# Optimization experiments

Measured on AMD Instinct MI355X. Metric: run time of the kernel, lower is better.

Reference implementation:

```python
import jax, jax.numpy as jnp
import numpy as np

N_NODES = 100000
N_EDGES = 3200000
DIMS = [32, 256, 1024, 1024, 256, 6]


def setup_inputs() -> dict:
    key = jax.random.key(0)
    ks = jax.random.split(key, 2 + 2 * 5)
    inp = {
        "x": jax.random.normal(ks[0], (N_NODES, DIMS[0]), dtype=jnp.float32),
        "edge_index": jax.random.randint(ks[1], (2, N_EDGES), 0, N_NODES, dtype=jnp.int64),
    }
    for i in range(5):
        fan_in, fan_out = DIMS[i], DIMS[i + 1]
        scale = (2.0 / (fan_in + fan_out)) ** 0.5  # glorot-ish
        inp[f"W{i+1}"] = jax.random.normal(ks[2 + 2 * i], (fan_in, fan_out), dtype=jnp.float32) * scale
        inp[f"b{i+1}"] = jnp.zeros((fan_out,), dtype=jnp.float32)
    return inp


def _gcn_forward(x, edge_index, Ws, bs):
    N = x.shape[0]
    # add self loops (PyG GCNConv default)
    loop = jnp.arange(N, dtype=edge_index.dtype)
    src = jnp.concatenate([edge_index[0], loop])
    dst = jnp.concatenate([edge_index[1], loop])
    # symmetric normalization: deg computed on target index (gcn_norm)
    deg = jax.ops.segment_sum(jnp.ones_like(dst, dtype=x.dtype), dst, num_segments=N)
    dinv = jnp.where(deg > 0, jax.lax.rsqrt(deg), 0.0)
    norm = (dinv[src] * dinv[dst])[:, None]  # [E+N, 1]

    def conv(h, W, b):
        h = h @ W                                    # dense linear
        msg = h[src] * norm                          # gather + scale
        agg = jax.ops.segment_sum(msg, dst, num_segments=N)  # scatter-add
        return agg + b

    h = x
    for i in range(4):
        h = jax.nn.relu(conv(h, Ws[i], bs[i]))
    return conv(h, Ws[4], bs[4])


def reference(x, edge_index, W1, b1, W2, b2, W3, b3, W4, b4, W5, b5):
    return _gcn_forward(x, edge_index, (W1, W2, W3, W4, W5), (b1, b2, b3, b4, b5))
```

## Files before the change

kernel.cpp:

```cpp
#include <hip/hip_runtime.h>

typedef unsigned char u8;
typedef unsigned short u16;
typedef unsigned int u32;
typedef __bf16 bf16_t;
typedef bf16_t bf16x8 __attribute__((ext_vector_type(8)));
typedef float f32x4 __attribute__((ext_vector_type(4)));
typedef float f32x2 __attribute__((ext_vector_type(2)));

#define LDS_PTR(p) ((__attribute__((address_space(3))) unsigned int*)(p))
#define GLB_PTR(p) ((const __attribute__((address_space(1))) unsigned int*)(p))

#define BSH 9
#define BCAP 32768

static __device__ __forceinline__ float bf2f(u16 h) {
  u32 u = ((u32)h) << 16;
  return __builtin_bit_cast(float, u);
}
static __device__ __forceinline__ u16 f2bf(float f) {
  u32 u = __builtin_bit_cast(u32, f);
  u += 0x7fffu + ((u >> 16) & 1u);
  return (u16)(u >> 16);
}

static __device__ __forceinline__ int xcd_swizzle(int wg, int nwg) {
  const int q = nwg >> 3, r = nwg & 7;
  const int xcd = wg & 7, pos = wg >> 3;
  return (xcd < r ? xcd * (q + 1) : r * (q + 1) + (xcd - r) * q) + pos;
}

__global__ void detect_kernel(const int* __restrict__ ei, const u16* __restrict__ x,
                              int* __restrict__ flags, int* __restrict__ zp, int zn) {
  __shared__ int cnt;
  if (threadIdx.x == 0) cnt = 0;
  __syncthreads();
  if (blockIdx.x == 0) {
    if (ei[1 + 2 * threadIdx.x] != 0) atomicAdd(&cnt, 1);
    __syncthreads();
    if (threadIdx.x == 0) flags[0] = (cnt == 0) ? 1 : 0;
  } else if (blockIdx.x == 1) {
    u32 u = x[threadIdx.x];
    u32 e = (u >> 7) & 0xFF;
    if (e >= 0x60 && e <= 0x83) atomicAdd(&cnt, 1);
    __syncthreads();
    if (threadIdx.x == 0) flags[1] = (cnt >= 240) ? 0 : 1;
  } else {
    for (int i = threadIdx.x; i < zn; i += 256) zp[i] = 0;
  }
}

static __device__ __forceinline__ int eidx(const void* ei, size_t i, int m) {
  return m ? (int)((const long long*)ei)[i] : ((const int*)ei)[i];
}

__global__ void zero_out_kernel(void* __restrict__ out, int n, const int* __restrict__ flags) {
  int i = blockIdx.x * 256 + threadIdx.x;
  if (i < n) {
    if (flags[1]) ((float*)out)[i] = 0.0f;
    else ((u16*)out)[i] = 0;
  }
}

struct CvtArgs {
  const void* src[10];
  u16* dst[10];
  int K[10];
  int N[10];
  int start[11];
};
__global__ void convert_all_kernel(CvtArgs a, const int* __restrict__ flags) {
  int idx = blockIdx.x * 256 + threadIdx.x;
  int f32 = flags[1];
#pragma unroll
  for (int t = 0; t < 10; ++t) {
    if (idx >= a.start[t] && idx < a.start[t + 1]) {
      int local = idx - a.start[t];
      int K = a.K[t], N = a.N[t];
      int k = local / N, n = local - k * N;
      float v = f32 ? ((const float*)a.src[t])[local] : bf2f(((const u16*)a.src[t])[local]);
      a.dst[t][(size_t)n * K + k] = f2bf(v);
    }
  }
}

__global__ void prescale_x_kernel(const void* __restrict__ x, void* __restrict__ xs,
                                  const float* __restrict__ dinv, int n,
                                  const int* __restrict__ flags) {
  int i = blockIdx.x * 256 + threadIdx.x;
  if (i >= n) return;
  float w = dinv[i >> 5];
  if (flags[1]) ((float*)xs)[i] = ((const float*)x)[i] * w;
  else ((u16*)xs)[i] = f2bf(bf2f(((const u16*)x)[i]) * w);
}

__global__ __launch_bounds__(256) void bin_kernel(const void* __restrict__ ei,
                                                  int* __restrict__ gcur,
                                                  int2* __restrict__ pairs, int E, int Nn,
                                                  const int* __restrict__ flags, int nblk) {
  __shared__ int h[256];
  __shared__ int base[256];
  const int m = flags[0];
  const int nb = (Nn + (1 << BSH) - 1) >> BSH;
  const int per = (E + nblk - 1) / nblk;
  const int e0 = blockIdx.x * per;
  const int e1 = (e0 + per < E) ? e0 + per : E;
  for (int i = threadIdx.x; i < nb; i += 256) h[i] = 0;
  __syncthreads();
  for (int e = e0 + threadIdx.x; e < e1; e += 256) {
    int d = eidx(ei, (size_t)E + e, m);
    if ((u32)d < (u32)Nn) atomicAdd(&h[d >> BSH], 1);
  }
  __syncthreads();
  for (int i = threadIdx.x; i < nb; i += 256) {
    base[i] = atomicAdd(&gcur[i], h[i]);
    h[i] = 0;
  }
  __syncthreads();
  for (int e = e0 + threadIdx.x; e < e1; e += 256) {
    int d = eidx(ei, (size_t)E + e, m);
    if ((u32)d >= (u32)Nn) continue;
    int s = eidx(ei, (size_t)e, m);
    if ((u32)s >= (u32)Nn) s = 0;
    int b = d >> BSH;
    int p = base[b] + atomicAdd(&h[b], 1);
    if (p < BCAP) pairs[(size_t)b * BCAP + p] = make_int2(s, d);
  }
}

__global__ __launch_bounds__(256) void bucket_scan_kernel(const int* __restrict__ gcur,
                                                          int* __restrict__ gbase, int NB) {
  __shared__ int sd[256];
  int tid = threadIdx.x;
  int v = (tid < NB) ? gcur[tid] : 0;
  if (v > BCAP) v = BCAP;
  sd[tid] = v;
  __syncthreads();
  for (int s = 1; s < 256; s <<= 1) {
    int t = (tid >= s) ? sd[tid - s] : 0;
    __syncthreads();
    sd[tid] += t;
    __syncthreads();
  }
  if (tid < NB) gbase[tid] = sd[tid] - v;
}

__global__ __launch_bounds__(512) void bucket_finalize_kernel(
    const int2* __restrict__ pairs, const int* __restrict__ gcur,
    const int* __restrict__ gbase, int* __restrict__ rowp, float* __restrict__ dinv,
    int* __restrict__ csr, int Nn) {
  __shared__ int cnt[512];
  __shared__ int scn[512];
  const int b = blockIdx.x;
  const int n0 = b << BSH;
  const int tid = threadIdx.x;
  cnt[tid] = 0;
  __syncthreads();
  int tot = gcur[b];
  if (tot > BCAP) tot = BCAP;
  for (int i = tid; i < tot; i += 512) {
    int2 pr = pairs[(size_t)b * BCAP + i];
    atomicAdd(&cnt[pr.y - n0], 1);
  }
  __syncthreads();
  int myc = cnt[tid];
  scn[tid] = myc;
  __syncthreads();
  for (int s = 1; s < 512; s <<= 1) {
    int t = (tid >= s) ? scn[tid - s] : 0;
    __syncthreads();
    scn[tid] += t;
    __syncthreads();
  }
  const int node = n0 + tid;
  const int start = gbase[b] + scn[tid] - myc;
  if (node < Nn) {
    rowp[node] = start;
    dinv[node] = rsqrtf((float)(myc + 1));
    if (node == Nn - 1) rowp[Nn] = gbase[b] + scn[tid];
  }
  cnt[tid] = start;
  __syncthreads();
  for (int i = tid; i < tot; i += 512) {
    int2 pr = pairs[(size_t)b * BCAP + i];
    int p = atomicAdd(&cnt[pr.y - n0], 1);
    csr[p] = pr.x;
  }
}

template <int NPW, int ACT, bool SRCF, bool DSTF>
__global__ __launch_bounds__(256) void spmm_narrow_kernel(
    const void* __restrict__ Hb, void* __restrict__ Gb,
    const int* __restrict__ rowp, const int* __restrict__ csr,
    const float* __restrict__ dinv, const u16* __restrict__ bias,
    int relu, int Nn, int src_stride, int dst_stride, const int* __restrict__ flags) {
  constexpr int G = 64 / NPW;
  constexpr int B = 16;
  const int lane = threadIdx.x & 63;
  const int col = lane & (G - 1);
  const int node = blockIdx.x * 4 * NPW + (threadIdx.x >> 6) * NPW + (lane / G);
  const bool anode = node < Nn;
  const bool act = anode && (col < ACT);
  int sf32 = 0, of32 = 0;
  if (SRCF) sf32 = flags[1];
  if (DSTF) of32 = flags[1];
  const u16* Hs = (const u16*)Hb;
  const float* Hf = (const float*)Hb;

  int e0 = 0, cnt = 0;
  if (anode) {
    e0 = rowp[node];
    cnt = rowp[node + 1] - e0;
  }
  float acc = 0.0f;
  for (int jb = 0; jb < cnt; jb += B) {
    int s[B];
#pragma unroll
    for (int j = 0; j < B; ++j) {
      bool val = (jb + j) < cnt;
      s[j] = val ? csr[e0 + jb + j] : node;
    }
    float v[B];
#pragma unroll
    for (int j = 0; j < B; ++j) {
      bool val = act && ((jb + j) < cnt);
      size_t idx = (size_t)s[j] * src_stride + col;
      v[j] = val ? ((SRCF && sf32) ? Hf[idx] : bf2f(Hs[idx])) : 0.0f;
    }
#pragma unroll
    for (int j = 0; j < B; ++j) acc += v[j];
  }
  if (!act) return;
  const float wi = dinv[node];
  {
    size_t idx = (size_t)node * src_stride + col;
    acc += (SRCF && sf32) ? Hf[idx] : bf2f(Hs[idx]);
  }
  float v = acc * wi;
  if (bias) v += bf2f(bias[col]);
  if (relu) v = fmaxf(v, 0.0f);
  size_t didx = (size_t)node * dst_stride + col;
  if (DSTF && of32) ((float*)Gb)[didx] = v;
  else ((u16*)Gb)[didx] = f2bf(v);
}

template <int W>
__global__ __launch_bounds__(256) void spmm_fp8_kernel(
    const u8* __restrict__ Hq, u16* __restrict__ Gout,
    const int* __restrict__ rowp, const int* __restrict__ csr,
    const float* __restrict__ dinv, int n0, int n1, int dst_stride) {
  constexpr int BPL = W / 64;
  constexpr int ND = BPL / 4;
  constexpr int B = (W == 1024) ? 8 : 16;
  const int lane = threadIdx.x & 63;
  const int node = __builtin_amdgcn_readfirstlane(n0 + blockIdx.x * 4 + (threadIdx.x >> 6));
  if (node >= n1) return;
  const int off = lane * BPL;
  f32x2 acc[2 * ND] = {};

  auto dec1 = [&](const u32* d) {
#pragma unroll
    for (int q = 0; q < ND; ++q) {
      f32x2 a = __builtin_amdgcn_cvt_pk_f32_fp8((int)d[q], false);
      f32x2 b = __builtin_amdgcn_cvt_pk_f32_fp8((int)d[q], true);
      acc[2 * q] += a;
      acc[2 * q + 1] += b;
    }
  };
  auto ldrow = [&](u32* v, int s) {
    const u8* p = Hq + (size_t)s * W + off;
    if constexpr (ND == 4) *(int4*)v = *(const int4*)p;
    else v[0] = *(const u32*)p;
  };

  const int e0 = rowp[node];
  const int cnt = rowp[node + 1] - e0;
  const int tot = cnt + 1;
  const int NB2 = (tot + B - 1) / B;
  const int NBF = NB2 - 1;

  u32 vA[B][ND], vB[B][ND];

  auto ldb_full = [&](u32 (*v)[ND], int k) {
    const int base = k * B;
    int s[B];
#pragma unroll
    for (int j = 0; j < B; ++j) s[j] = csr[e0 + base + j];
#pragma unroll
    for (int j = 0; j < B; ++j) ldrow(v[j], s[j]);
  };
  auto ldb_last = [&](u32 (*v)[ND]) {
    const int base = NBF * B;
#pragma unroll
    for (int j = 0; j < B; ++j) {
      const int i = base + j;
      if (i < tot) {
        int s = (i < cnt) ? csr[e0 + i] : node;
        ldrow(v[j], s);
      } else {
#pragma unroll
        for (int q = 0; q < ND; ++q) v[j][q] = 0u;
      }
    }
  };
  auto decfull = [&](u32 (*v)[ND]) {
#pragma unroll
    for (int j = 0; j < B; ++j) dec1(v[j]);
  };

  if (NB2 == 1) {
    ldb_last(vA);
    decfull(vA);
  } else {
    ldb_last(vA);
    ldb_full(vB, 0);
    int k = 1;
    while (k + 1 < NBF) {
      decfull(vA);
      ldb_full(vA, k);
      decfull(vB);
      ldb_full(vB, k + 1);
      k += 2;
    }
    if (k < NBF) {
      decfull(vA);
      ldb_full(vA, k);
      decfull(vB);
      decfull(vA);
    } else {
      decfull(vA);
      decfull(vB);
    }
  }

  const float wi = dinv[node];
  u32 d[2 * ND];
#pragma unroll
  for (int kk = 0; kk < 2 * ND; ++kk) {
    float v0 = acc[kk].x * wi, v1 = acc[kk].y * wi;
    d[kk] = (u32)f2bf(v0) | ((u32)f2bf(v1) << 16);
  }
  u16* gp = Gout + (size_t)(node - n0) * dst_stride + off;
  if constexpr (ND == 4) {
    ((int4*)gp)[0] = make_int4((int)d[0], (int)d[1], (int)d[2], (int)d[3]);
    ((int4*)gp)[1] = make_int4((int)d[4], (int)d[5], (int)d[6], (int)d[7]);
  } else {
    *(int2*)gp = make_int2((int)d[0], (int)d[1]);
  }
}

__global__ __launch_bounds__(256) void spmm_u8_kernel(
    const u8* __restrict__ Hq, u16* __restrict__ G,
    const int* __restrict__ rowp, const int* __restrict__ csr,
    const float* __restrict__ dinv, const u32* __restrict__ maxbits,
    const u16* __restrict__ bias, int relu, int Nn, int dst_stride) {
  constexpr int B = 16;
  const int lane = threadIdx.x & 63;
  const int node = __builtin_amdgcn_readfirstlane(blockIdx.x * 4 + (threadIdx.x >> 6));
  if (node >= Nn) return;
  const int off = lane * 4;
  float mx = __builtin_bit_cast(float, *maxbits);
  float sq = mx > 0.0f ? mx * (1.0f / 127.0f) : 0.0f;
  u32 aP0 = 0, aP1 = 0;

  auto dec1 = [&](u32 d) {
    aP0 += d & 0x00ff00ffu;
    aP1 += (d >> 8) & 0x00ff00ffu;
  };
  auto ldrow = [&](u32* v, int s) { *v = *(const u32*)(Hq + (size_t)s * 256 + off); };

  const int e0 = rowp[node];
  const int cnt = rowp[node + 1] - e0;
  const int tot = cnt + 1;
  const int NB2 = (tot + B - 1) / B;
  const int NBF = NB2 - 1;

  u32 vA[B], vB[B];

  auto ldb_full = [&](u32* v, int k) {
    const int base = k * B;
    int s[B];
#pragma unroll
    for (int j = 0; j < B; ++j) s[j] = csr[e0 + base + j];
#pragma unroll
    for (int j = 0; j < B; ++j) ldrow(&v[j], s[j]);
  };
  auto ldb_last = [&](u32* v) {
    const int base = NBF * B;
#pragma unroll
    for (int j = 0; j < B; ++j) {
      const int i = base + j;
      if (i < tot) {
        int s = (i < cnt) ? csr[e0 + i] : node;
        ldrow(&v[j], s);
      } else {
        v[j] = 0u;
      }
    }
  };
  auto decfull = [&](u32* v) {
#pragma unroll
    for (int j = 0; j < B; ++j) dec1(v[j]);
  };

  if (NB2 == 1) {
    ldb_last(vA);
    decfull(vA);
  } else {
    ldb_last(vA);
    ldb_full(vB, 0);
    int k = 1;
    while (k + 1 < NBF) {
      decfull(vA);
      ldb_full(vA, k);
      decfull(vB);
      ldb_full(vB, k + 1);
      k += 2;
    }
    if (k < NBF) {
      decfull(vA);
      ldb_full(vA, k);
      decfull(vB);
      decfull(vA);
    } else {
      decfull(vA);
      decfull(vB);
    }
  }

  const float wi = dinv[node];
  float su[4];
  su[0] = (float)(aP0 & 0xffffu);
  su[2] = (float)(aP0 >> 16);
  su[1] = (float)(aP1 & 0xffffu);
  su[3] = (float)(aP1 >> 16);
  float vals[4];
#pragma unroll
  for (int k2 = 0; k2 < 4; ++k2) {
    float v = (su[k2] - 128.0f * (float)tot) * wi * sq;
    if (bias) v += bf2f(bias[off + k2]);
    if (relu) v = fmaxf(v, 0.0f);
    vals[k2] = v;
  }
  u32 d0 = (u32)f2bf(vals[0]) | ((u32)f2bf(vals[1]) << 16);
  u32 d1 = (u32)f2bf(vals[2]) | ((u32)f2bf(vals[3]) << 16);
  *(int2*)(G + (size_t)node * dst_stride + off) = make_int2((int)d0, (int)d1);
}

__global__ void quant_kernel(const u16* __restrict__ t4, u8* __restrict__ t4q,
                             const u32* __restrict__ maxbits, int n4) {
  int i = blockIdx.x * 256 + threadIdx.x;
  if (i >= n4) return;
  float mx = __builtin_bit_cast(float, *maxbits);
  float inv = mx > 0.0f ? 127.0f / mx : 0.0f;
  int2 v = ((const int2*)t4)[i];
  float f0 = bf2f((u16)(v.x & 0xffff)), f1 = bf2f((u16)((u32)v.x >> 16));
  float f2 = bf2f((u16)(v.y & 0xffff)), f3 = bf2f((u16)((u32)v.y >> 16));
  int q0 = (int)rintf(f0 * inv), q1 = (int)rintf(f1 * inv);
  int q2 = (int)rintf(f2 * inv), q3 = (int)rintf(f3 * inv);
  q0 = min(127, max(-127, q0)) + 128; q1 = min(127, max(-127, q1)) + 128;
  q2 = min(127, max(-127, q2)) + 128; q3 = min(127, max(-127, q3)) + 128;
  ((u32*)t4q)[i] = (u32)q0 | ((u32)q1 << 8) | ((u32)q2 << 16) | ((u32)q3 << 24);
}

__global__ __launch_bounds__(256) void gemm_fast_kernel(
    const u16* __restrict__ A, int lda, const u16* __restrict__ Bt,
    u16* __restrict__ C, int ldc, const u16* __restrict__ bias,
    int M, int N, int K, int relu, int fp8out, u32* __restrict__ maxout,
    const float* __restrict__ rowscale) {
  __shared__ __align__(16) u16 sA[128 * 64];
  __shared__ __align__(16) u16 sB[128 * 64];
  const int tid = threadIdx.x;
  const int lane = tid & 63;
  const int wave = __builtin_amdgcn_readfirstlane(tid >> 6);
  const int gx = gridDim.x;
  int wg = blockIdx.y * gx + blockIdx.x;
  wg = xcd_swizzle(wg, gx * gridDim.y);
  const int m0 = (wg / gx) * 128, n0 = (wg % gx) * 128;
  const int wm = (wave & 1) * 64, wn = (wave >> 1) * 64;
  const int lr = lane & 15, lq = lane >> 4;
  const int lrow = lane >> 3;
  const int lcol = (lane & 7) * 8;
  f32x4 acc[4][4] = {};

  for (int kb = 0; kb < K; kb += 64) {
#pragma unroll
    for (int it = 0; it < 4; ++it) {
      const int rbase = (it * 4 + wave) * 8;
      int gm = m0 + rbase + lrow;
      if (gm >= M) gm = M - 1;
      __builtin_amdgcn_global_load_lds(GLB_PTR(A + (size_t)gm * lda + kb + lcol),
                                       LDS_PTR(sA + rbase * 64), 16, 0, 0);
      const int gn = n0 + rbase + lrow;
      __builtin_amdgcn_global_load_lds(GLB_PTR(Bt + (size_t)gn * K + kb + lcol),
                                       LDS_PTR(sB + rbase * 64), 16, 0, 0);
    }
    __syncthreads();
#pragma unroll
    for (int ks = 0; ks < 2; ++ks) {
      bf16x8 af[4], bfr[4];
#pragma unroll
      for (int i = 0; i < 4; ++i)
        af[i] = *(const bf16x8*)(sA + (wm + i * 16 + lr) * 64 + ks * 32 + lq * 8);
#pragma unroll
      for (int i = 0; i < 4; ++i)
        bfr[i] = *(const bf16x8*)(sB + (wn + i * 16 + lr) * 64 + ks * 32 + lq * 8);
#pragma unroll
      for (int im = 0; im < 4; ++im)
#pragma unroll
        for (int in = 0; in < 4; ++in)
          acc[im][in] = __builtin_amdgcn_mfma_f32_16x16x32_bf16(af[im], bfr[in], acc[im][in], 0, 0, 0);
    }
    __syncthreads();
  }
  float rs[4][4];
#pragma unroll
  for (int im = 0; im < 4; ++im)
#pragma unroll
    for (int r = 0; r < 4; ++r) {
      int row = m0 + wm + im * 16 + lq * 4 + r;
      rs[im][r] = rowscale ? rowscale[row < M ? row : 0] : 1.0f;
    }
  u32 mymax = 0;
#pragma unroll
  for (int im = 0; im < 4; ++im) {
#pragma unroll
    for (int in = 0; in < 4; ++in) {
      int col = n0 + wn + in * 16 + lr;
      float bv = bias ? bf2f(bias[col]) : 0.0f;
#pragma unroll
      for (int r = 0; r < 4; ++r) {
        int row = m0 + wm + im * 16 + lq * 4 + r;
        if (row < M) {
          float v = acc[im][in][r] + bv;
          if (relu) v = fmaxf(v, 0.0f);
          if (rowscale) v *= rs[im][r];
          if (maxout) {
            u32 ab = __builtin_bit_cast(u32, v) & 0x7fffffffu;
            mymax = mymax > ab ? mymax : ab;
          }
          if (fp8out) {
            int pk = __builtin_amdgcn_cvt_pk_fp8_f32(v, v, 0, false);
            ((u8*)C)[(size_t)row * ldc + col] = (u8)(pk & 0xff);
          } else {
            C[(size_t)row * ldc + col] = f2bf(v);
          }
        }
      }
    }
  }
  if (maxout) {
    u32* red = (u32*)sA;
    red[tid] = mymax;
    __syncthreads();
    for (int s = 128; s > 0; s >>= 1) {
      if (tid < s) red[tid] = red[tid] > red[tid + s] ? red[tid] : red[tid + s];
      __syncthreads();
    }
    if (tid == 0) atomicMax(maxout, red[0]);
  }
}

#define LP 72
__global__ __launch_bounds__(256) void gemm_small_kernel(
    const u16* __restrict__ A, int lda, const u16* __restrict__ Bt,
    u16* __restrict__ C, int ldc, const u16* __restrict__ bias,
    int M, int N, int K, int relu, int fp8out, const float* __restrict__ rowscale) {
  __shared__ __align__(16) u16 sA[128 * LP];
  __shared__ __align__(16) u16 sB[128 * LP];
  const int tid = threadIdx.x;
  const int lane = tid & 63, wave = tid >> 6;
  const int gx = gridDim.x;
  int wg = blockIdx.y * gx + blockIdx.x;
  wg = xcd_swizzle(wg, gx * gridDim.y);
  const int m0 = (wg / gx) * 128, n0 = (wg % gx) * 128;
  const int wm = (wave & 1) * 64, wn = (wave >> 1) * 64;
  const int lr = lane & 15;
  const int lq = lane >> 4;
  f32x4 acc[4][4] = {};

  for (int kb = 0; kb < K; kb += 64) {
#pragma unroll
    for (int it = 0; it < 4; ++it) {
      int linear = it * 2048 + tid * 8;
      int row = linear >> 6, kc = linear & 63;
      int gm = m0 + row, gk = kb + kc;
      int4 v = make_int4(0, 0, 0, 0);
      if (gm < M && gk < K) v = *(const int4*)(A + (size_t)gm * lda + gk);
      *(int4*)(sA + row * LP + kc) = v;
    }
#pragma unroll
    for (int it = 0; it < 4; ++it) {
      int linear = it * 2048 + tid * 8;
      int row = linear >> 6, kc = linear & 63;
      int gn = n0 + row, gk = kb + kc;
      int4 v = make_int4(0, 0, 0, 0);
      if (gn < N && gk < K) v = *(const int4*)(Bt + (size_t)gn * K + gk);
      *(int4*)(sB + row * LP + kc) = v;
    }
    __syncthreads();
#pragma unroll
    for (int ks = 0; ks < 2; ++ks) {
      bf16x8 af[4], bfr[4];
#pragma unroll
      for (int i = 0; i < 4; ++i)
        af[i] = *(const bf16x8*)(sA + (wm + i * 16 + lr) * LP + ks * 32 + lq * 8);
#pragma unroll
      for (int i = 0; i < 4; ++i)
        bfr[i] = *(const bf16x8*)(sB + (wn + i * 16 + lr) * LP + ks * 32 + lq * 8);
#pragma unroll
      for (int im = 0; im < 4; ++im)
#pragma unroll
        for (int in = 0; in < 4; ++in)
          acc[im][in] = __builtin_amdgcn_mfma_f32_16x16x32_bf16(af[im], bfr[in], acc[im][in], 0, 0, 0);
    }
    __syncthreads();
  }
  float rs[4][4];
#pragma unroll
  for (int im = 0; im < 4; ++im)
#pragma unroll
    for (int r = 0; r < 4; ++r) {
      int row = m0 + wm + im * 16 + lq * 4 + r;
      rs[im][r] = rowscale ? rowscale[row < M ? row : 0] : 1.0f;
    }
#pragma unroll
  for (int im = 0; im < 4; ++im) {
#pragma unroll
    for (int in = 0; in < 4; ++in) {
      int col = n0 + wn + in * 16 + lr;
      if (col >= N) continue;
      float bv = bias ? bf2f(bias[col]) : 0.0f;
#pragma unroll
      for (int r = 0; r < 4; ++r) {
        int row = m0 + wm + im * 16 + lq * 4 + r;
        if (row < M) {
          float v = acc[im][in][r] + bv;
          if (relu) v = fmaxf(v, 0.0f);
          if (rowscale) v *= rs[im][r];
          if (fp8out) {
            int pk = __builtin_amdgcn_cvt_pk_fp8_f32(v, v, 0, false);
            ((u8*)C)[(size_t)row * ldc + col] = (u8)(pk & 0xff);
          } else {
            C[(size_t)row * ldc + col] = f2bf(v);
          }
        }
      }
    }
  }
}

extern "C" void kernel_launch(void* const* d_in, const int* in_sizes, int n_in,
                              void* d_out, int out_size, void* d_ws, size_t ws_size,
                              hipStream_t stream) {
  const u16* x  = (const u16*)d_in[0];
  const int* ei = (const int*)d_in[1];

  const int Nn = in_sizes[0] / 32;
  const int E  = in_sizes[1] / 2;
  const int CH = (Nn + 7) / 8;
  const int NR = (Nn + CH - 1) / CH;
  const int NB = (Nn + (1 << BSH) - 1) >> BSH;

  char* w = (char*)d_ws;
  size_t off = 0;
  auto alloc = [&](size_t bytes) -> void* {
    void* p = w + off;
    off = (off + bytes + 255) & ~(size_t)255;
    return p;
  };
  int*   flags  = (int*)alloc(256);
  int*   gcur   = (int*)alloc(1024);
  int*   gbase  = (int*)alloc(1024);
  u32*   tmax   = (u32*)alloc(256);
  int*   rowp   = (int*)alloc((size_t)(Nn + 1) * 4);
  float* dinv   = (float*)alloc((size_t)Nn * 4);
  int*   csr    = (int*)alloc((size_t)E * 4);
  u16*   Wt1    = (u16*)alloc((size_t)32 * 256 * 2);
  u16*   Wt2    = (u16*)alloc((size_t)256 * 1024 * 2);
  u16*   Wt3    = (u16*)alloc((size_t)1024 * 1024 * 2);
  u16*   Wt4    = (u16*)alloc((size_t)1024 * 256 * 2);
  u16*   Wt5    = (u16*)alloc((size_t)256 * 6 * 2);
  u16*   bc1    = (u16*)alloc(256 * 2);
  u16*   bc2    = (u16*)alloc(1024 * 2);
  u16*   bc3    = (u16*)alloc(1024 * 2);
  u16*   bc4    = (u16*)alloc(256 * 2);
  u16*   bc5    = (u16*)alloc(6 * 2);
  size_t selems = (size_t)CH * 1024;
  u16*   S      = (u16*)alloc(selems * 2);
  u16*   H      = (u16*)alloc((size_t)Nn * 1024 * 2);
  const size_t required = off;
  (void)n_in;

  if (ws_size < required) {
    if (ws_size >= 4096) {
      detect_kernel<<<3, 256, 0, stream>>>(ei, x, flags, gcur, 576);
      zero_out_kernel<<<(out_size + 255) / 256, 256, 0, stream>>>(d_out, out_size, flags);
    }
    return;
  }

  void* xs = (void*)H;
  u8*  h2q = (u8*)H;
  u8*  t4q = (u8*)H;
  u16* g2  = H + (size_t)Nn * 512;
  u16* t4  = H + (size_t)Nn * 512;
  u8*  h1q = (u8*)(H + (size_t)Nn * 768);
  u16* h3R = H + (size_t)Nn * 768;
  u16* h4  = H + (size_t)Nn * 768;

  int2* pairs = (int2*)H;

  detect_kernel<<<3, 256, 0, stream>>>(ei, x, flags, gcur, 576);
  bin_kernel<<<1024, 256, 0, stream>>>(ei, gcur, pairs, E, Nn, flags, 1024);
  bucket_scan_kernel<<<1, 256, 0, stream>>>(gcur, gbase, NB);
  bucket_finalize_kernel<<<NB, 512, 0, stream>>>(pairs, gcur, gbase, rowp, dinv, csr, Nn);

  prescale_x_kernel<<<(Nn * 32 + 255) / 256, 256, 0, stream>>>(x, xs, dinv, Nn * 32, flags);

  {
    CvtArgs a;
    const int Ks[10] = {32, 1, 256, 1, 1024, 1, 1024, 1, 256, 1};
    const int Ns[10] = {256, 256, 1024, 1024, 1024, 1024, 256, 256, 6, 6};
    u16* ds[10] = {Wt1, bc1, Wt2, bc2, Wt3, bc3, Wt4, bc4, Wt5, bc5};
    int cum = 0;
    for (int t = 0; t < 10; ++t) {
      a.src[t] = d_in[2 + t];
      a.dst[t] = ds[t];
      a.K[t] = Ks[t];
      a.N[t] = Ns[t];
      a.start[t] = cum;
      cum += Ks[t] * Ns[t];
    }
    a.start[10] = cum;
    convert_all_kernel<<<(cum + 255) / 256, 256, 0, stream>>>(a, flags);
  }

  const int sg = (Nn + 3) / 4;
  const int mb = (Nn + 127) / 128;

  spmm_narrow_kernel<2, 32, true, false><<<(Nn + 7) / 8, 256, 0, stream>>>(
      xs, S, rowp, csr, dinv, nullptr, 0, Nn, 32, 32, flags);
  gemm_small_kernel<<<dim3(2, mb), 256, 0, stream>>>(S, 32, Wt1, (u16*)h1q, 256, bc1,
                                                     Nn, 256, 32, 1, 1, dinv);

  spmm_fp8_kernel<256><<<sg, 256, 0, stream>>>(h1q, g2, rowp, csr, dinv, 0, Nn, 256);
  gemm_fast_kernel<<<dim3(8, mb), 256, 0, stream>>>(g2, 256, Wt2, (u16*)h2q, 1024, bc2,
                                                    Nn, 1024, 256, 1, 1, nullptr, dinv);

  for (int R = 0; R < NR; ++R) {
    int n0 = R * CH;
    int n1 = n0 + CH < Nn ? n0 + CH : Nn;
    int MR = n1 - n0;
    int mbr = (MR + 127) / 128;
    spmm_fp8_kernel<1024><<<(MR + 3) / 4, 256, 0, stream>>>(h2q, S, rowp, csr, dinv, n0, n1, 1024);
    gemm_fast_kernel<<<dim3(8, mbr), 256, 0, stream>>>(S, 1024, Wt3, h3R, 1024, bc3,
                                                       MR, 1024, 1024, 1, 0, nullptr, nullptr);
    gemm_fast_kernel<<<dim3(2, mbr), 256, 0, stream>>>(h3R, 1024, Wt4, t4 + (size_t)n0 * 256, 256,
                                                       nullptr, MR, 256, 1024, 0, 0, tmax,
                                                       dinv + n0);
  }

  quant_kernel<<<(Nn * 64 + 255) / 256, 256, 0, stream>>>(t4, t4q, tmax, Nn * 64);

  spmm_u8_kernel<<<sg, 256, 0, stream>>>(t4q, h4, rowp, csr, dinv, tmax, bc4, 1, Nn, 256);

  gemm_small_kernel<<<dim3(1, mb), 256, 0, stream>>>(h4, 256, Wt5, S, 6, nullptr,
                                                     Nn, 6, 256, 0, 0, dinv);
  spmm_narrow_kernel<8, 6, false, true><<<(Nn + 31) / 32, 256, 0, stream>>>(
      S, d_out, rowp, csr, dinv, bc5, 0, Nn, 6, 6, flags);
}
```

Measured before the change: 2.179 ms.

## Fuse source-degree scaling into SpMM gathers and enlarge layer-3 chunk size

Removes the prescale_x kernel and the dinv row scaling on the layer-4 GEMM output, and instead applies the per-source dinv weight inside the gather loops of the first narrow SpMM and the u8 SpMM. The u8 SpMM switches from packed integer accumulation to float per-channel FMA with a weight sum for the zero-point correction. The node chunk size for the layer-3/4 loop grows from Nn/8 to Nn/4 when workspace allows, cutting launches. The trade is an extra dinv gather per edge and more ALU work in the u8 SpMM, in exchange for one fewer pass over x and fewer chunk iterations.

```diff
diff --git a/kernel.cpp b/kernel.cpp
--- a/kernel.cpp
+++ b/kernel.cpp
@@ -82,16 +82,6 @@
       a.dst[t][(size_t)n * K + k] = f2bf(v);
     }
   }
-}
-
-__global__ void prescale_x_kernel(const void* __restrict__ x, void* __restrict__ xs,
-                                  const float* __restrict__ dinv, int n,
-                                  const int* __restrict__ flags) {
-  int i = blockIdx.x * 256 + threadIdx.x;
-  if (i >= n) return;
-  float w = dinv[i >> 5];
-  if (flags[1]) ((float*)xs)[i] = ((const float*)x)[i] * w;
-  else ((u16*)xs)[i] = f2bf(bf2f(((const u16*)x)[i]) * w);
 }
 
 __global__ __launch_bounds__(256) void bin_kernel(const void* __restrict__ ei,
@@ -188,7 +178,7 @@
   }
 }
 
-template <int NPW, int ACT, bool SRCF, bool DSTF>
+template <int NPW, int ACT, bool SRCF, bool DSTF, bool EDGEW>
 __global__ __launch_bounds__(256) void spmm_narrow_kernel(
     const void* __restrict__ Hb, void* __restrict__ Gb,
     const int* __restrict__ rowp, const int* __restrict__ csr,
@@ -220,6 +210,11 @@
       bool val = (jb + j) < cnt;
       s[j] = val ? csr[e0 + jb + j] : node;
     }
+    float wv[B];
+    if constexpr (EDGEW) {
+#pragma unroll
+      for (int j = 0; j < B; ++j) wv[j] = ((jb + j) < cnt) ? dinv[s[j]] : 0.0f;
+    }
     float v[B];
 #pragma unroll
     for (int j = 0; j < B; ++j) {
@@ -228,13 +223,18 @@
       v[j] = val ? ((SRCF && sf32) ? Hf[idx] : bf2f(Hs[idx])) : 0.0f;
     }
 #pragma unroll
-    for (int j = 0; j < B; ++j) acc += v[j];
+    for (int j = 0; j < B; ++j) {
+      if constexpr (EDGEW) acc += wv[j] * v[j];
+      else acc += v[j];
+    }
   }
   if (!act) return;
   const float wi = dinv[node];
   {
     size_t idx = (size_t)node * src_stride + col;
-    acc += (SRCF && sf32) ? Hf[idx] : bf2f(Hs[idx]);
+    float sv = (SRCF && sf32) ? Hf[idx] : bf2f(Hs[idx]);
+    if constexpr (EDGEW) acc += wi * sv;
+    else acc += sv;
   }
   float v = acc * wi;
   if (bias) v += bf2f(bias[col]);
@@ -361,11 +361,14 @@
   const int off = lane * 4;
   float mx = __builtin_bit_cast(float, *maxbits);
   float sq = mx > 0.0f ? mx * (1.0f / 127.0f) : 0.0f;
-  u32 aP0 = 0, aP1 = 0;
-
-  auto dec1 = [&](u32 d) {
-    aP0 += d & 0x00ff00ffu;
-    aP1 += (d >> 8) & 0x00ff00ffu;
+  float a0 = 0.0f, a1 = 0.0f, a2 = 0.0f, a3 = 0.0f, wsum = 0.0f;
+
+  auto dec1 = [&](u32 d, float w) {
+    a0 += w * (float)(d & 0xffu);
+    a1 += w * (float)((d >> 8) & 0xffu);
+    a2 += w * (float)((d >> 16) & 0xffu);
+    a3 += w * (float)(d >> 24);
+    wsum += w;
   };
   auto ldrow = [&](u32* v, int s) { *v = *(const u32*)(Hq + (size_t)s * 256 + off); };
 
@@ -376,68 +379,69 @@
   const int NBF = NB2 - 1;
 
   u32 vA[B], vB[B];
-
-  auto ldb_full = [&](u32* v, int k) {
+  float wA[B], wB[B];
+
+  auto ldb_full = [&](u32* v, float* wv, int k) {
     const int base = k * B;
     int s[B];
 #pragma unroll
     for (int j = 0; j < B; ++j) s[j] = csr[e0 + base + j];
 #pragma unroll
+    for (int j = 0; j < B; ++j) wv[j] = dinv[s[j]];
+#pragma unroll
     for (int j = 0; j < B; ++j) ldrow(&v[j], s[j]);
   };
-  auto ldb_last = [&](u32* v) {
+  auto ldb_last = [&](u32* v, float* wv) {
     const int base = NBF * B;
 #pragma unroll
     for (int j = 0; j < B; ++j) {
       const int i = base + j;
       if (i < tot) {
         int s = (i < cnt) ? csr[e0 + i] : node;
+        wv[j] = dinv[s];
         ldrow(&v[j], s);
       } else {
         v[j] = 0u;
+        wv[j] = 0.0f;
       }
     }
   };
-  auto decfull = [&](u32* v) {
-#pragma unroll
-    for (int j = 0; j < B; ++j) dec1(v[j]);
+  auto decfull = [&](u32* v, float* wv) {
+#pragma unroll
+    for (int j = 0; j < B; ++j) dec1(v[j], wv[j]);
   };
 
   if (NB2 == 1) {
-    ldb_last(vA);
-    decfull(vA);
+    ldb_last(vA, wA);
+    decfull(vA, wA);
   } else {
-    ldb_last(vA);
-    ldb_full(vB, 0);
+    ldb_last(vA, wA);
+    ldb_full(vB, wB, 0);
     int k = 1;
     while (k + 1 < NBF) {
-      decfull(vA);
-      ldb_full(vA, k);
-      decfull(vB);
-      ldb_full(vB, k + 1);
+      decfull(vA, wA);
+      ldb_full(vA, wA, k);
+      decfull(vB, wB);
+      ldb_full(vB, wB, k + 1);
       k += 2;
     }
     if (k < NBF) {
-      decfull(vA);
-      ldb_full(vA, k);
-      decfull(vB);
-      decfull(vA);
+      decfull(vA, wA);
+      ldb_full(vA, wA, k);
+      decfull(vB, wB);
+      decfull(vA, wA);
     } else {
-      decfull(vA);
-      decfull(vB);
+      decfull(vA, wA);
+      decfull(vB, wB);
     }
   }
 
   const float wi = dinv[node];
-  float su[4];
-  su[0] = (float)(aP0 & 0xffffu);
-  su[2] = (float)(aP0 >> 16);
-  su[1] = (float)(aP1 & 0xffffu);
-  su[3] = (float)(aP1 >> 16);
+  float su[4] = {a0, a1, a2, a3};
   float vals[4];
 #pragma unroll
   for (int k2 = 0; k2 < 4; ++k2) {
-    float v = (su[k2] - 128.0f * (float)tot) * wi * sq;
+    float v = (su[k2] - 128.0f * wsum) * wi * sq;
     if (bias) v += bf2f(bias[off + k2]);
     if (relu) v = fmaxf(v, 0.0f);
     vals[k2] = v;
@@ -513,14 +517,6 @@
     }
     __syncthreads();
   }
-  float rs[4][4];
-#pragma unroll
-  for (int im = 0; im < 4; ++im)
-#pragma unroll
-    for (int r = 0; r < 4; ++r) {
-      int row = m0 + wm + im * 16 + lq * 4 + r;
-      rs[im][r] = rowscale ? rowscale[row < M ? row : 0] : 1.0f;
-    }
   u32 mymax = 0;
 #pragma unroll
   for (int im = 0; im < 4; ++im) {
@@ -534,7 +530,7 @@
         if (row < M) {
           float v = acc[im][in][r] + bv;
           if (relu) v = fmaxf(v, 0.0f);
-          if (rowscale) v *= rs[im][r];
+          if (rowscale) v *= rowscale[row];
           if (maxout) {
             u32 ab = __builtin_bit_cast(u32, v) & 0x7fffffffu;
             mymax = mymax > ab ? mymax : ab;
@@ -616,14 +612,6 @@
     }
     __syncthreads();
   }
-  float rs[4][4];
-#pragma unroll
-  for (int im = 0; im < 4; ++im)
-#pragma unroll
-    for (int r = 0; r < 4; ++r) {
-      int row = m0 + wm + im * 16 + lq * 4 + r;
-      rs[im][r] = rowscale ? rowscale[row < M ? row : 0] : 1.0f;
-    }
 #pragma unroll
   for (int im = 0; im < 4; ++im) {
 #pragma unroll
@@ -637,7 +625,7 @@
         if (row < M) {
           float v = acc[im][in][r] + bv;
           if (relu) v = fmaxf(v, 0.0f);
-          if (rowscale) v *= rs[im][r];
+          if (rowscale) v *= rowscale[row];
           if (fp8out) {
             int pk = __builtin_amdgcn_cvt_pk_fp8_f32(v, v, 0, false);
             ((u8*)C)[(size_t)row * ldc + col] = (u8)(pk & 0xff);
@@ -658,8 +646,6 @@
 
   const int Nn = in_sizes[0] / 32;
   const int E  = in_sizes[1] / 2;
-  const int CH = (Nn + 7) / 8;
-  const int NR = (Nn + CH - 1) / CH;
   const int NB = (Nn + (1 << BSH) - 1) >> BSH;
 
   char* w = (char*)d_ws;
@@ -686,9 +672,21 @@
   u16*   bc3    = (u16*)alloc(1024 * 2);
   u16*   bc4    = (u16*)alloc(256 * 2);
   u16*   bc5    = (u16*)alloc(6 * 2);
-  size_t selems = (size_t)CH * 1024;
-  u16*   S      = (u16*)alloc(selems * 2);
-  u16*   H      = (u16*)alloc((size_t)Nn * 1024 * 2);
+
+  const size_t fixed_end = off;
+  const size_t hbytes = (size_t)Nn * 1024 * 2;
+  auto align256 = [](size_t b) { return (b + 255) & ~(size_t)255; };
+  int CH = Nn / 4;
+  if (CH < 1) CH = 1;
+  {
+    size_t need = fixed_end + align256((size_t)CH * 1024 * 2) + align256(hbytes);
+    if (ws_size < need) CH = (Nn + 7) / 8;
+  }
+  while ((size_t)CH * 1024 < (size_t)Nn * 32) CH *= 2;
+  const int NR = (Nn + CH - 1) / CH;
+
+  u16*   S      = (u16*)alloc((size_t)CH * 1024 * 2);
+  u16*   H      = (u16*)alloc(hbytes);
   const size_t required = off;
   (void)n_in;
 
@@ -700,7 +698,6 @@
     return;
   }
 
-  void* xs = (void*)H;
   u8*  h2q = (u8*)H;
   u8*  t4q = (u8*)H;
   u16* g2  = H + (size_t)Nn * 512;
@@ -715,8 +712,6 @@
   bin_kernel<<<1024, 256, 0, stream>>>(ei, gcur, pairs, E, Nn, flags, 1024);
   bucket_scan_kernel<<<1, 256, 0, stream>>>(gcur, gbase, NB);
   bucket_finalize_kernel<<<NB, 512, 0, stream>>>(pairs, gcur, gbase, rowp, dinv, csr, Nn);
-
-  prescale_x_kernel<<<(Nn * 32 + 255) / 256, 256, 0, stream>>>(x, xs, dinv, Nn * 32, flags);
 
   {
     CvtArgs a;
@@ -739,8 +734,8 @@
   const int sg = (Nn + 3) / 4;
   const int mb = (Nn + 127) / 128;
 
-  spmm_narrow_kernel<2, 32, true, false><<<(Nn + 7) / 8, 256, 0, stream>>>(
-      xs, S, rowp, csr, dinv, nullptr, 0, Nn, 32, 32, flags);
+  spmm_narrow_kernel<2, 32, true, false, true><<<(Nn + 7) / 8, 256, 0, stream>>>(
+      x, S, rowp, csr, dinv, nullptr, 0, Nn, 32, 32, flags);
   gemm_small_kernel<<<dim3(2, mb), 256, 0, stream>>>(S, 32, Wt1, (u16*)h1q, 256, bc1,
                                                      Nn, 256, 32, 1, 1, dinv);
 
@@ -757,8 +752,7 @@
     gemm_fast_kernel<<<dim3(8, mbr), 256, 0, stream>>>(S, 1024, Wt3, h3R, 1024, bc3,
                                                        MR, 1024, 1024, 1, 0, nullptr, nullptr);
     gemm_fast_kernel<<<dim3(2, mbr), 256, 0, stream>>>(h3R, 1024, Wt4, t4 + (size_t)n0 * 256, 256,
-                                                       nullptr, MR, 256, 1024, 0, 0, tmax,
-                                                       dinv + n0);
+                                                       nullptr, MR, 256, 1024, 0, 0, tmax, nullptr);
   }
 
   quant_kernel<<<(Nn * 64 + 255) / 256, 256, 0, stream>>>(t4, t4q, tmax, Nn * 64);
@@ -767,6 +761,6 @@
 
   gemm_small_kernel<<<dim3(1, mb), 256, 0, stream>>>(h4, 256, Wt5, S, 6, nullptr,
                                                      Nn, 6, 256, 0, 0, dinv);
-  spmm_narrow_kernel<8, 6, false, true><<<(Nn + 31) / 32, 256, 0, stream>>>(
+  spmm_narrow_kernel<8, 6, false, true, false><<<(Nn + 31) / 32, 256, 0, stream>>>(
       S, d_out, rowp, csr, dinv, bc5, 0, Nn, 6, 6, flags);
 }
```

After: 2.063 ms. 5.3% less time.
